# Kernel optimization log

Hardware: AMD Instinct MI355X
Metric: run time of the kernel (lower is better)

The kernel has to match this reference:

```python
import jax, jax.numpy as jnp
import numpy as np

# World configuration (2D layout ['h','w'])
B = 16            # batch
NH, NW = 64, 64   # token grid (token_sizes)
DO = 768          # dim_in + dim_coords
KH, KW = 16, 16   # kernel_sizes (patch extent, overlapping)
SH, SW = 8, 8     # patch_sizes (strides)
H, WF = 512, 512  # field_sizes
E = H * WF        # world.num_elements


def _build_fold_index():
    # idx[h, w, dh, dw] = clamp(h*SH+dh, 0, H-1)*WF + clamp(w*SW+dw, 0, WF-1)
    # mirrors FieldDecoder._build_fold_index with grid strides (WF, 1)
    ph = np.clip(np.arange(NH)[:, None] * SH + np.arange(KH)[None, :], 0, H - 1)   # [NH,KH]
    pw = np.clip(np.arange(NW)[:, None] * SW + np.arange(KW)[None, :], 0, WF - 1)  # [NW,KW]
    idx = ph[:, None, :, None] * WF + pw[None, :, None, :]                          # [NH,NW,KH,KW]
    return jnp.asarray(idx.reshape(-1), dtype=jnp.int32)


def setup_inputs() -> dict:
    key = jax.random.key(0)
    k1, k2 = jax.random.split(key)
    tgt = jax.random.normal(k1, (B, NH * NW, DO), dtype=jnp.float32)
    weight = jax.random.normal(k2, (KH, KW, DO), dtype=jnp.float32) * 0.02  # EinMix weight (k=v=1 absorbed)
    idx = _build_fold_index()
    return {"tgt": tgt, "weight": weight, "idx": idx}


def reference(tgt, weight, idx):
    # EinMix: 'b (h w) do -> b (h w hh ww)'  (shared per-patch projection, k=v=1)
    proj = jnp.einsum('bnd,xyd->bnxy', tgt, weight)          # [B, NH*NW, KH, KW]
    proj = proj.reshape(B, -1)                                # flat order (h, w, hh, ww) == idx layout
    # scatter_reduce(reduce='mean', include_self=False): sum then divide by counts
    sums = jnp.zeros((B, E), proj.dtype).at[:, idx].add(proj)
    counts = jnp.zeros((E,), proj.dtype).at[idx].add(1.0)     # every element is covered (kernel >= stride)
    field = sums / jnp.maximum(counts, 1.0)
    # unflatten_fields: 'b (flat) -> b h w'
    return field.reshape(B, H, WF)
```

## Files before the change

### kernel.cpp

```cpp
#include <hip/hip_runtime.h>
#include <hip/hip_bf16.h>

#define DIM      768
#define NPATCH   4096
#define BATCH    16
#define MROWS    65536
#define NCOLS    256

typedef __attribute__((ext_vector_type(8))) short bf16x8;
typedef __attribute__((ext_vector_type(4))) float f32x4;

static __device__ __forceinline__ unsigned short f2bf(float f) {
    union { float f; unsigned int u; } v; v.f = f;
    unsigned int u = v.u;
    return (unsigned short)((u + 0x7FFFu + ((u >> 16) & 1u)) >> 16);
}
static __device__ __forceinline__ float bf2f(unsigned int u16) {
    union { unsigned int i; float f; } x; x.i = u16 << 16; return x.f;
}
static __device__ __forceinline__ bf16x8 pack_bf8(float4 a, float4 b) {
    union { bf16x8 v; unsigned int u[4]; } r;
    r.u[0] = (unsigned)f2bf(a.x) | ((unsigned)f2bf(a.y) << 16);
    r.u[1] = (unsigned)f2bf(a.z) | ((unsigned)f2bf(a.w) << 16);
    r.u[2] = (unsigned)f2bf(b.x) | ((unsigned)f2bf(b.y) << 16);
    r.u[3] = (unsigned)f2bf(b.z) | ((unsigned)f2bf(b.w) << 16);
    return r.v;
}

__global__ void wpack_kernel(const float* __restrict__ w, unsigned short* __restrict__ wf) {
    const int t    = blockIdx.x * blockDim.x + threadIdx.x;
    const int lane = t & 63;
    const int j    = (t >> 6) & 15;
    const int kk   = t >> 10;
    const int n    = j * 16 + (lane & 15);
    const int k    = kk * 32 + (lane >> 4) * 8;
    const float* src = w + (size_t)n * DIM + k;
    float4 v0 = *(const float4*)src;
    float4 v1 = *(const float4*)(src + 4);
    union { bf16x8 v; uint4 q; } o;
    o.v = pack_bf8(v0, v1);
    *(uint4*)(wf + (size_t)t * 8) = o.q;
}

__global__ __launch_bounds__(256, 2) void gemm_kernel(const float* __restrict__ A,
                                                      const unsigned short* __restrict__ Bf,
                                                      unsigned short* __restrict__ Cb) {
    __shared__ unsigned short smem[128 * 256];

    const int tid  = threadIdx.x;
    const int w    = tid >> 6;
    const int lane = tid & 63;
    const int l15  = lane & 15;
    const int quad = lane >> 4;
    const int m0   = blockIdx.x * 128;

    f32x4 acc[2][16] = {};

    const float* a0 = A + (size_t)(m0 + w * 32 + l15) * DIM + quad * 8;
    const float* a1 = a0 + (size_t)16 * DIM;

    for (int c = 0; c < 6; ++c) {
        __syncthreads();
        {
            const uint4* src = (const uint4*)Bf + c * 4096 + tid;
            uint4* dst = (uint4*)smem + tid;
            #pragma unroll 4
            for (int s = 0; s < 16; ++s)
                dst[s * 256] = src[s * 256];
        }
        __syncthreads();

        #pragma unroll
        for (int kk = 0; kk < 4; ++kk) {
            const int kg = c * 4 + kk;
            const float4 r00 = *(const float4*)(a0 + kg * 32);
            const float4 r01 = *(const float4*)(a0 + kg * 32 + 4);
            const float4 r10 = *(const float4*)(a1 + kg * 32);
            const float4 r11 = *(const float4*)(a1 + kg * 32 + 4);
            const bf16x8 af0 = pack_bf8(r00, r01);
            const bf16x8 af1 = pack_bf8(r10, r11);
            #pragma unroll
            for (int j = 0; j < 16; ++j) {
                const bf16x8 b = *(const bf16x8*)(smem + ((kk * 16 + j) * 64 + lane) * 8);
                acc[0][j] = __builtin_amdgcn_mfma_f32_16x16x32_bf16(af0, b, acc[0][j], 0, 0, 0);
                acc[1][j] = __builtin_amdgcn_mfma_f32_16x16x32_bf16(af1, b, acc[1][j], 0, 0, 0);
            }
        }
    }

    __syncthreads();
    #pragma unroll
    for (int i = 0; i < 2; ++i)
        #pragma unroll
        for (int j = 0; j < 16; ++j)
            #pragma unroll
            for (int rr = 0; rr < 4; ++rr)
                smem[(w * 32 + i * 16 + quad * 4 + rr) * 256 + j * 16 + l15] = f2bf(acc[i][j][rr]);
    __syncthreads();

    const int orow = tid >> 3;
    const int ou   = tid & 7;
    #pragma unroll
    for (int rb = 0; rb < 4; ++rb) {
        const int row = orow + rb * 32;
        const unsigned short* src = smem + row * 256 + ou * 32;
        unsigned short* dst = Cb + (size_t)(m0 + row) * NCOLS + ou * 32;
        #pragma unroll
        for (int q = 0; q < 4; ++q)
            *(uint4*)(dst + q * 8) = *(const uint4*)(src + q * 8);
    }
}

#define CSTRG 280
#define PSTRG 152
__global__ __launch_bounds__(256, 2) void gather_kernel(const unsigned short* __restrict__ proj,
                                                        float* __restrict__ out) {
    __shared__ unsigned short sCur[64 * CSTRG];
    __shared__ unsigned short sPrevHi[64 * PSTRG];

    const int blk = blockIdx.x;
    const int b   = blk >> 6;
    const int h   = blk & 63;
    const int tid = threadIdx.x;
    const unsigned short* base = proj + (size_t)b * (NPATCH * NCOLS);

    const uint4* gCur = (const uint4*)(base + (size_t)h * 64 * 256);
    #pragma unroll
    for (int p = 0; p < 8; ++p) {
        const int i = tid + p * 256;
        *(uint4*)(sCur + (i >> 5) * CSTRG + (i & 31) * 8) = gCur[i];
    }
    if (h > 0) {
        const uint4* gPrev = (const uint4*)(base + (size_t)(h - 1) * 64 * 256);
        #pragma unroll
        for (int p = 0; p < 4; ++p) {
            const int i = tid + p * 256;
            *(uint4*)(sPrevHi + (i >> 4) * PSTRG + (i & 15) * 8) = gPrev[(i >> 4) * 32 + 16 + (i & 15)];
        }
    }
    __syncthreads();

    const float fch_base = (h == 0) ? 1.f : 0.5f;

    #pragma unroll
    for (int t = 0; t < 2; ++t) {
        const int task = tid + t * 256;
        const int r  = task >> 6;
        const int wg = task & 63;
        const int ph = h * 8 + r;

        float s[8] = {0.f, 0.f, 0.f, 0.f, 0.f, 0.f, 0.f, 0.f};
        auto addq = [&](uint4 v) {
            const unsigned int u[4] = {v.x, v.y, v.z, v.w};
            #pragma unroll
            for (int q = 0; q < 4; ++q) {
                s[2 * q]     += bf2f(u[q] & 0xFFFFu);
                s[2 * q + 1] += bf2f(u[q] >> 16);
            }
        };
        auto sumq = [&](uint4 v) -> float {
            const unsigned int u[4] = {v.x, v.y, v.z, v.w};
            float e = 0.f;
            #pragma unroll
            for (int q = 0; q < 4; ++q) e += bf2f(u[q] & 0xFFFFu) + bf2f(u[q] >> 16);
            return e;
        };

        addq(*(const uint4*)(sCur + wg * CSTRG + r * 16));
        if (wg > 0) addq(*(const uint4*)(sCur + (wg - 1) * CSTRG + r * 16 + 8));
        if (h > 0) {
            addq(*(const uint4*)(sPrevHi + wg * PSTRG + r * 16));
            if (wg > 0) addq(*(const uint4*)(sPrevHi + (wg - 1) * PSTRG + r * 16 + 8));
        }
        if (wg == 63) {
            s[7] += sumq(*(const uint4*)(sCur + 63 * CSTRG + r * 16 + 8));
            if (h > 0) s[7] += sumq(*(const uint4*)(sPrevHi + 63 * PSTRG + r * 16 + 8));
        }
        float fch = fch_base;
        if (ph == 511) {
            fch = 0.1f;
            #pragma unroll 1
            for (int dh = 8; dh < 16; ++dh) {
                addq(*(const uint4*)(sCur + wg * CSTRG + dh * 16));
                if (wg > 0) addq(*(const uint4*)(sCur + (wg - 1) * CSTRG + dh * 16 + 8));
                if (wg == 63) s[7] += sumq(*(const uint4*)(sCur + 63 * CSTRG + dh * 16 + 8));
            }
        }

        const float fcw = (wg == 0) ? 1.f : 0.5f;
        float f7 = fcw;
        if (wg == 63) f7 = 0.1f;
        float* orow = out + ((size_t)(b * 512 + ph)) * 512 + wg * 8;
        *(float4*)orow       = make_float4(s[0] * fch * fcw, s[1] * fch * fcw,
                                           s[2] * fch * fcw, s[3] * fch * fcw);
        *(float4*)(orow + 4) = make_float4(s[4] * fch * fcw, s[5] * fch * fcw,
                                           s[6] * fch * fcw, s[7] * fch * f7);
    }
}

extern "C" void kernel_launch(void* const* d_in, const int* in_sizes, int n_in,
                              void* d_out, int out_size, void* d_ws, size_t ws_size,
                              hipStream_t stream) {
    const float* tgt    = (const float*)d_in[0];
    const float* weight = (const float*)d_in[1];
    float* out = (float*)d_out;

    unsigned short* proj = (unsigned short*)d_ws;
    unsigned short* wf   = (unsigned short*)((char*)d_ws + (size_t)MROWS * NCOLS * 2);

    wpack_kernel<<<96, 256, 0, stream>>>(weight, wf);
    gemm_kernel<<<MROWS / 128, 256, 0, stream>>>(tgt, wf, proj);
    gather_kernel<<<BATCH * 64, 256, 0, stream>>>(proj, out);
}
```

Baseline: 322.6 us.

## Double-buffer B tiles via global_load_lds and prefetch A into registers

The GEMM K loop is restructured into 12 steps of 64, with the weight tile for the next step loaded straight into a second LDS buffer through global_load_lds. The A rows for the next step are prefetched into registers while MFMAs run on the current buffer. This replaces the old load-sync-compute pattern, which had two barriers per chunk, and aims to hide global latency behind compute. The epilogue LDS writes also get an XOR swizzle on the column block to reduce bank conflicts, with the readback adjusted to match. A single barrier per step guards buffer reuse, so correctness depends on the async LDS loads completing before that barrier.

```diff
diff --git a/kernel.cpp b/kernel.cpp
--- a/kernel.cpp
+++ b/kernel.cpp
@@ -25,6 +25,11 @@
     r.u[2] = (unsigned)f2bf(b.x) | ((unsigned)f2bf(b.y) << 16);
     r.u[3] = (unsigned)f2bf(b.z) | ((unsigned)f2bf(b.w) << 16);
     return r.v;
+}
+
+static __device__ __forceinline__ void gload16(const void* g, void* l) {
+    __builtin_amdgcn_global_load_lds((const __attribute__((address_space(1))) void*)g,
+                                     (__attribute__((address_space(3))) void*)l, 16, 0, 0);
 }
 
 __global__ void wpack_kernel(const float* __restrict__ w, unsigned short* __restrict__ wf) {
@@ -58,44 +63,64 @@
 
     const float* a0 = A + (size_t)(m0 + w * 32 + l15) * DIM + quad * 8;
     const float* a1 = a0 + (size_t)16 * DIM;
-
-    for (int c = 0; c < 6; ++c) {
+    const uint4* gB = (const uint4*)Bf;
+
+    #pragma unroll
+    for (int s = 0; s < 8; ++s)
+        gload16(gB + s * 256 + tid, smem + (size_t)(s * 256 + tid) * 8);
+    float4 rA[8];
+    #pragma unroll
+    for (int kk2 = 0; kk2 < 2; ++kk2) {
+        rA[kk2 * 4 + 0] = *(const float4*)(a0 + kk2 * 32);
+        rA[kk2 * 4 + 1] = *(const float4*)(a0 + kk2 * 32 + 4);
+        rA[kk2 * 4 + 2] = *(const float4*)(a1 + kk2 * 32);
+        rA[kk2 * 4 + 3] = *(const float4*)(a1 + kk2 * 32 + 4);
+    }
+    __syncthreads();
+
+    for (int t = 0; t < 12; ++t) {
+        bf16x8 af[4];
+        #pragma unroll
+        for (int kk2 = 0; kk2 < 2; ++kk2) {
+            af[kk2 * 2 + 0] = pack_bf8(rA[kk2 * 4 + 0], rA[kk2 * 4 + 1]);
+            af[kk2 * 2 + 1] = pack_bf8(rA[kk2 * 4 + 2], rA[kk2 * 4 + 3]);
+        }
+        if (t + 1 < 12) {
+            const uint4* src = gB + (t + 1) * 2048;
+            unsigned short* dstb = smem + ((t + 1) & 1) * 16384;
+            #pragma unroll
+            for (int s = 0; s < 8; ++s)
+                gload16(src + s * 256 + tid, dstb + (size_t)(s * 256 + tid) * 8);
+            const int col = (t + 1) * 64;
+            #pragma unroll
+            for (int kk2 = 0; kk2 < 2; ++kk2) {
+                rA[kk2 * 4 + 0] = *(const float4*)(a0 + col + kk2 * 32);
+                rA[kk2 * 4 + 1] = *(const float4*)(a0 + col + kk2 * 32 + 4);
+                rA[kk2 * 4 + 2] = *(const float4*)(a1 + col + kk2 * 32);
+                rA[kk2 * 4 + 3] = *(const float4*)(a1 + col + kk2 * 32 + 4);
+            }
+        }
+        const unsigned short* bbase = smem + (t & 1) * 16384;
+        #pragma unroll
+        for (int kk2 = 0; kk2 < 2; ++kk2) {
+            #pragma unroll
+            for (int j = 0; j < 16; ++j) {
+                const bf16x8 b = *(const bf16x8*)(bbase + ((kk2 * 16 + j) * 64 + lane) * 8);
+                acc[0][j] = __builtin_amdgcn_mfma_f32_16x16x32_bf16(af[kk2 * 2 + 0], b, acc[0][j], 0, 0, 0);
+                acc[1][j] = __builtin_amdgcn_mfma_f32_16x16x32_bf16(af[kk2 * 2 + 1], b, acc[1][j], 0, 0, 0);
+            }
+        }
         __syncthreads();
-        {
-            const uint4* src = (const uint4*)Bf + c * 4096 + tid;
-            uint4* dst = (uint4*)smem + tid;
-            #pragma unroll 4
-            for (int s = 0; s < 16; ++s)
-                dst[s * 256] = src[s * 256];
-        }
-        __syncthreads();
-
-        #pragma unroll
-        for (int kk = 0; kk < 4; ++kk) {
-            const int kg = c * 4 + kk;
-            const float4 r00 = *(const float4*)(a0 + kg * 32);
-            const float4 r01 = *(const float4*)(a0 + kg * 32 + 4);
-            const float4 r10 = *(const float4*)(a1 + kg * 32);
-            const float4 r11 = *(const float4*)(a1 + kg * 32 + 4);
-            const bf16x8 af0 = pack_bf8(r00, r01);
-            const bf16x8 af1 = pack_bf8(r10, r11);
-            #pragma unroll
-            for (int j = 0; j < 16; ++j) {
-                const bf16x8 b = *(const bf16x8*)(smem + ((kk * 16 + j) * 64 + lane) * 8);
-                acc[0][j] = __builtin_amdgcn_mfma_f32_16x16x32_bf16(af0, b, acc[0][j], 0, 0, 0);
-                acc[1][j] = __builtin_amdgcn_mfma_f32_16x16x32_bf16(af1, b, acc[1][j], 0, 0, 0);
-            }
-        }
-    }
-
-    __syncthreads();
+    }
+
     #pragma unroll
     for (int i = 0; i < 2; ++i)
         #pragma unroll
         for (int j = 0; j < 16; ++j)
             #pragma unroll
             for (int rr = 0; rr < 4; ++rr)
-                smem[(w * 32 + i * 16 + quad * 4 + rr) * 256 + j * 16 + l15] = f2bf(acc[i][j][rr]);
+                smem[(w * 32 + i * 16 + quad * 4 + rr) * 256 + ((j ^ quad) * 16 + l15)] =
+                    f2bf(acc[i][j][rr]);
     __syncthreads();
 
     const int orow = tid >> 3;
@@ -103,11 +128,14 @@
     #pragma unroll
     for (int rb = 0; rb < 4; ++rb) {
         const int row = orow + rb * 32;
-        const unsigned short* src = smem + row * 256 + ou * 32;
+        const int rq  = (row >> 2) & 3;
+        const unsigned short* srcrow = smem + row * 256;
         unsigned short* dst = Cb + (size_t)(m0 + row) * NCOLS + ou * 32;
         #pragma unroll
-        for (int q = 0; q < 4; ++q)
-            *(uint4*)(dst + q * 8) = *(const uint4*)(src + q * 8);
+        for (int q = 0; q < 4; ++q) {
+            const int off = (ou * 32 + q * 8) ^ (rq * 16);
+            *(uint4*)(dst + q * 8) = *(const uint4*)(srcrow + off);
+        }
     }
 }
 
```

New measurement: 313.7 us. -2.8%, faster.
